# Kernel optimization log

Measured on AMD Instinct MI355X. Metric: run time of the kernel, lower is better.

Reference implementation:

```python
import jax, jax.numpy as jnp
import numpy as np

N_NODES = 100000
N_EDGES = 1600000
HID = 64
EDIM = 32


def _linear_params(key, fan_in, fan_out):
    # torch.nn.Linear default init: U(-1/sqrt(fan_in), 1/sqrt(fan_in))
    kw, kb = jax.random.split(key)
    bound = 1.0 / np.sqrt(fan_in)
    w = jax.random.uniform(kw, (fan_in, fan_out), jnp.float32, -bound, bound)
    b = jax.random.uniform(kb, (fan_out,), jnp.float32, -bound, bound)
    return w, b


def setup_inputs() -> dict:
    key = jax.random.key(0)
    ks = jax.random.split(key, 7)
    x = jax.random.normal(ks[0], (N_NODES, HID), jnp.float32)
    edge_index = jax.random.randint(ks[1], (2, N_EDGES), 0, N_NODES, jnp.int64)
    edge_attr = jax.random.normal(ks[2], (N_EDGES, EDIM), jnp.float32)
    ew1, eb1 = _linear_params(ks[3], 2 * HID + EDIM, HID)
    ew2, eb2 = _linear_params(ks[4], HID, HID)
    nw1, nb1 = _linear_params(ks[5], 2 * HID, HID)
    nw2, nb2 = _linear_params(ks[6], HID, HID)
    return {
        "x": x, "edge_index": edge_index, "edge_attr": edge_attr,
        "ew1": ew1, "eb1": eb1, "ew2": ew2, "eb2": eb2,
        "nw1": nw1, "nb1": nb1, "nw2": nw2, "nb2": nb2,
    }


def reference(x, edge_index, edge_attr, ew1, eb1, ew2, eb2, nw1, nb1, nw2, nb2):
    row, col = edge_index[0], edge_index[1]
    # gather endpoint features + edge attrs -> [E, 2*HID + EDIM]
    edge_features = jnp.concatenate([x[row], x[col], edge_attr], axis=-1)
    # edge MLP
    h = jax.nn.relu(edge_features @ ew1 + eb1)
    messages = h @ ew2 + eb2  # [E, HID]
    # scatter-add into source nodes (index_add_ on row)
    aggregated = jax.ops.segment_sum(messages, row, num_segments=x.shape[0])
    # node MLP
    out = jnp.concatenate([x, aggregated], axis=-1)
    out = jax.nn.relu(out @ nw1 + nb1)
    out = out @ nw2 + nb2
    return out
```

## Files before the change

kernel.cpp:

```cpp
#include <hip/hip_runtime.h>
#include <hip/hip_bf16.h>


#define TPB 256
#define MAXD 64
#define EDGE_BLOCKS 2048
#define SCAT_BLOCKS 2048
#define PREP_BLOCKS 1024
#define NODE_BLOCKS 1024

typedef float v2f __attribute__((ext_vector_type(2)));
typedef float v4f __attribute__((ext_vector_type(4)));
typedef __attribute__((ext_vector_type(8))) short s8v;
typedef __attribute__((ext_vector_type(4))) float f4v;
typedef __attribute__((ext_vector_type(4))) unsigned int u4v;
typedef unsigned int uint32;

#define SEG32(SRC, NCH, KB, W, COL, ACC)                                \
  for (int kc_ = 0; kc_ < (NCH); ++kc_) {                               \
    const float4 a_ = ((const float4*)(SRC))[kc_];                      \
    const float av_[4] = {a_.x, a_.y, a_.z, a_.w};                      \
    _Pragma("unroll")                                                   \
    for (int j_ = 0; j_ < 4; ++j_) {                                    \
      const float ak_ = av_[j_];                                        \
      const float* wr_ = (W) + ((KB) + kc_ * 4 + j_) * 64 + (COL);      \
      _Pragma("unroll")                                                 \
      for (int cc_ = 0; cc_ < 32; ++cc_)                                \
        ACC[cc_] = fmaf(ak_, wr_[cc_], ACC[cc_]);                       \
    }                                                                   \
  }

__device__ __forceinline__ uint32 pk_bf16(float a, float b) {
  uint32 ua = __float_as_uint(a);
  uint32 ub = __float_as_uint(b);
  ua = ua + 0x7FFFu + ((ua >> 16) & 1u);
  ub = ub + 0x7FFFu + ((ub >> 16) & 1u);
  return (ub & 0xFFFF0000u) | (ua >> 16);
}

__device__ __forceinline__ short f2bf(float f) {
  uint32 u = __float_as_uint(f);
  u = u + 0x7FFFu + ((u >> 16) & 1u);
  return (short)(u >> 16);
}


__global__ __launch_bounds__(TPB)
void k_scatter3(const int* __restrict__ ei, int* __restrict__ cnt,
                int2* __restrict__ ec, int E) {
  const int stride = gridDim.x * TPB;
  for (int e = blockIdx.x * TPB + threadIdx.x; e < E; e += stride) {
    const int r = ei[e];
    const int c = ei[E + e];
    int k = atomicAdd(&cnt[r], 1);
    if (k < MAXD) ec[(size_t)r * MAXD + k] = make_int2(e, c);
  }
}


__global__ __launch_bounds__(TPB)
void k_prep4(const float* __restrict__ x,
             const float* __restrict__ ew1, const float* __restrict__ eb1,
             float* __restrict__ U, float* __restrict__ V, int N)
{
  const int lane = threadIdx.x & 63;
  const int wid  = __builtin_amdgcn_readfirstlane(threadIdx.x >> 6);
  const int nunits = 4 * ((N + 63) / 64);
  const int wstride = gridDim.x * 4;

  for (int unit = blockIdx.x * 4 + wid; unit < nunits; unit += wstride) {
    const int q = unit & 3;
    const int n = (unit >> 2) * 64 + lane;
    if (n >= N) continue;

    const int uv = q >> 1;
    const int h = (q & 1) * 32;
    const float* W = ew1 + uv * 64 * 64;

    float acc[32];
    if (uv) {
      #pragma unroll
      for (int j = 0; j < 32; ++j) acc[j] = 0.f;
    } else {
      #pragma unroll
      for (int j = 0; j < 32; ++j) acc[j] = eb1[h + j];
    }
    SEG32(x + (size_t)n * 64, 16, 0, W, h, acc)

    float* dst = (uv ? V : U) + (size_t)n * 64 + h;
    float4* d4 = (float4*)dst;
    #pragma unroll
    for (int c4 = 0; c4 < 8; ++c4)
      d4[c4] = make_float4(acc[c4*4+0], acc[c4*4+1], acc[c4*4+2], acc[c4*4+3]);
  }
}


__global__ __launch_bounds__(TPB, 4)
void k_edge_mfma2(const float* __restrict__ U, const float* __restrict__ V,
                  const float* __restrict__ ea, const int2* __restrict__ ec,
                  const float* __restrict__ ew1,
                  const int* __restrict__ cnt,
                  float* __restrict__ H, int N)
{
  const int lane = threadIdx.x & 63;
  const int wid  = __builtin_amdgcn_readfirstlane(threadIdx.x >> 6);
  const int m16  = lane & 15;
  const int g4   = lane >> 4;

  s8v bfrag[4];
  #pragma unroll
  for (int t = 0; t < 4; ++t) {
    #pragma unroll
    for (int j = 0; j < 8; ++j)
      bfrag[t][j] = f2bf(ew1[(128 + g4 * 8 + j) * 64 + t * 16 + m16]);
  }
  asm volatile("" : "+v"(bfrag[0]), "+v"(bfrag[1]),
                    "+v"(bfrag[2]), "+v"(bfrag[3]));

  const int wstride = gridDim.x * 4;

  for (int n = blockIdx.x * 4 + wid; n < N; n += wstride) {
    int d = __builtin_amdgcn_readfirstlane(cnt[n]);
    d = (d < MAXD) ? d : MAXD;

    float uvv[4];
    #pragma unroll
    for (int t = 0; t < 4; ++t) uvv[t] = U[(size_t)n * 64 + t * 16 + m16];

    const int2* ecp = ec + (size_t)n * MAXD;
    float hs[4] = {0.f, 0.f, 0.f, 0.f};
    const int ntile = (d + 15) >> 4;

    for (int tile = 0; tile < ntile; ++tile) {
      const int sbase = tile * 16;

      const bool rowok = (sbase + m16) < d;
      const int eidr = rowok ? ecp[sbase + m16].x : 0;

      const float4* ear = (const float4*)(ea + (size_t)eidr * 32 + g4 * 8);
      const float4 fa = ear[0];
      const float4 fb = ear[1];
      u4v ua;
      ua.x = pk_bf16(fa.x, fa.y);
      ua.y = pk_bf16(fa.z, fa.w);
      ua.z = pk_bf16(fb.x, fb.y);
      ua.w = pk_bf16(fb.z, fb.w);
      const s8v afrag = __builtin_bit_cast(s8v, ua);

      const int4 c01 = *(const int4*)(ecp + sbase + g4 * 4);
      const int4 c23 = *(const int4*)(ecp + sbase + g4 * 4 + 2);
      const int ca[4] = {c01.y, c01.w, c23.y, c23.w};
      const int rg0 = sbase + g4 * 4;

      #pragma unroll
      for (int t = 0; t < 4; ++t) {
        f4v dd = __builtin_amdgcn_mfma_f32_16x16x32_bf16(
            afrag, bfrag[t], (f4v){0.f, 0.f, 0.f, 0.f}, 0, 0, 0);
        const int ch = t * 16 + m16;
        #pragma unroll
        for (int j = 0; j < 4; ++j) {
          const int rg = rg0 + j;
          const int cs = (rg < d) ? ca[j] : 0;
          const float vvv = V[(size_t)cs * 64 + ch];
          const float h = fmaxf(dd[j] + uvv[t] + vvv, 0.f);
          hs[t] += (rg < d) ? h : 0.f;
        }
      }
    }

    #pragma unroll
    for (int t = 0; t < 4; ++t) {
      hs[t] += __shfl_xor(hs[t], 16);
      hs[t] += __shfl_xor(hs[t], 32);
    }

    float hv = hs[0];
    hv = (g4 == 1) ? hs[1] : hv;
    hv = (g4 == 2) ? hs[2] : hv;
    hv = (g4 == 3) ? hs[3] : hv;
    H[(size_t)n * 64 + g4 * 16 + m16] = hv;
  }
}


__global__ __launch_bounds__(TPB)
void k_node4(const float* __restrict__ x, const float* __restrict__ Hin,
             const int* __restrict__ deg,
             const float* __restrict__ ew2, const float* __restrict__ eb2,
             const float* __restrict__ nw1, const float* __restrict__ nb1,
             const float* __restrict__ nw2, const float* __restrict__ nb2,
             float* __restrict__ out, int N)
{
  __shared__ float sb[2][64 * 65];

  const int tid  = threadIdx.x;
  const int wv   = __builtin_amdgcn_readfirstlane(tid >> 6);
  const int lane = tid & 63;
  const int grp  = wv >> 1;
  const int h    = (wv & 1) * 32;

  for (int base = blockIdx.x * 128; base < N; base += gridDim.x * 128) {
    const int n  = base + grp * 64 + lane;
    const bool valid = (n < N);
    const int nn = valid ? n : (N - 1);

    float* srow = &sb[grp][lane * 65];

    float acc[32];
    const float dg = (float)min(deg[nn], MAXD);
    #pragma unroll
    for (int j = 0; j < 32; ++j) acc[j] = dg * eb2[h + j];
    SEG32(Hin + (size_t)nn * 64, 16, 0, ew2, h, acc)

    #pragma unroll
    for (int j = 0; j < 32; ++j) srow[h + j] = acc[j];
    __syncthreads();

    float bcc[32];
    #pragma unroll
    for (int j = 0; j < 32; ++j) bcc[j] = nb1[h + j];
    SEG32(x + (size_t)nn * 64, 16, 0, nw1, h, bcc)
    for (int k = 0; k < 64; ++k) {
      const float ak = srow[k];
      const float* wr = nw1 + (64 + k) * 64 + h;
      #pragma unroll
      for (int cc = 0; cc < 32; ++cc) bcc[cc] = fmaf(ak, wr[cc], bcc[cc]);
    }
    __syncthreads();

    #pragma unroll
    for (int j = 0; j < 32; ++j) srow[h + j] = fmaxf(bcc[j], 0.f);
    __syncthreads();

    float occ[32];
    #pragma unroll
    for (int j = 0; j < 32; ++j) occ[j] = nb2[h + j];
    for (int k = 0; k < 64; ++k) {
      const float ak = srow[k];
      const float* wr = nw2 + k * 64 + h;
      #pragma unroll
      for (int cc = 0; cc < 32; ++cc) occ[cc] = fmaf(ak, wr[cc], occ[cc]);
    }

    if (valid) {
      float4* ov = (float4*)(out + (size_t)n * 64 + h);
      #pragma unroll
      for (int c4 = 0; c4 < 8; ++c4)
        ov[c4] = make_float4(occ[c4*4+0], occ[c4*4+1], occ[c4*4+2], occ[c4*4+3]);
    }
    __syncthreads();
  }
}


extern "C" void kernel_launch(void* const* d_in, const int* in_sizes, int n_in,
                              void* d_out, int out_size, void* d_ws, size_t ws_size,
                              hipStream_t stream) {
  const float* x   = (const float*)d_in[0];
  const int*   ei  = (const int*)d_in[1];
  const float* ea  = (const float*)d_in[2];
  const float* ew1 = (const float*)d_in[3];
  const float* eb1 = (const float*)d_in[4];
  const float* ew2 = (const float*)d_in[5];
  const float* eb2 = (const float*)d_in[6];
  const float* nw1 = (const float*)d_in[7];
  const float* nb1 = (const float*)d_in[8];
  const float* nw2 = (const float*)d_in[9];
  const float* nb2 = (const float*)d_in[10];
  float* out = (float*)d_out;

  const int N = in_sizes[0] / 64;
  const int E = in_sizes[1] / 2;

  float* U   = (float*)d_ws;
  float* V   = U + (size_t)N * 64;
  int* cnt   = (int*)(V + (size_t)N * 64);
  int2* ec   = (int2*)(cnt + N);
  float* H   = out;

  hipMemsetAsync(cnt, 0, (size_t)N * sizeof(int), stream);

  k_scatter3<<<SCAT_BLOCKS, TPB, 0, stream>>>(ei, cnt, ec, E);

  k_prep4<<<PREP_BLOCKS, TPB, 0, stream>>>(x, ew1, eb1, U, V, N);

  k_edge_mfma2<<<EDGE_BLOCKS, TPB, 0, stream>>>(
      U, V, ea, ec, ew1, cnt, H, N);

  k_node4<<<NODE_BLOCKS, TPB, 0, stream>>>(
      x, H, cnt, ew2, eb2, nw1, nb1, nw2, nb2, out, N);
}
```

Before: 325.2 us.

## Fuse edge bucketing scatter and U/V node precompute into one launch

Merges the edge bucketing kernel and the per-node U/V projection kernel into a single launch. Block roles are interleaved: two of every three blocks do the atomic scatter of edges into per-row buckets, and the third computes the U/V projections. The scatter loop also processes four edges per thread with loads and atomics batched to expose more memory parallelism. The aim is to overlap the atomic-heavy scatter with the compute-bound projection and save one launch, at the cost of role divergence within the grid.

Measured after the change: 316.8 us. 2.6% less time.

```diff
diff --git a/kernel.cpp b/kernel.cpp
--- a/kernel.cpp
+++ b/kernel.cpp
@@ -46,52 +46,75 @@
 
 
 __global__ __launch_bounds__(TPB)
-void k_scatter3(const int* __restrict__ ei, int* __restrict__ cnt,
-                int2* __restrict__ ec, int E) {
-  const int stride = gridDim.x * TPB;
-  for (int e = blockIdx.x * TPB + threadIdx.x; e < E; e += stride) {
-    const int r = ei[e];
-    const int c = ei[E + e];
-    int k = atomicAdd(&cnt[r], 1);
-    if (k < MAXD) ec[(size_t)r * MAXD + k] = make_int2(e, c);
-  }
-}
-
-
-__global__ __launch_bounds__(TPB)
-void k_prep4(const float* __restrict__ x,
-             const float* __restrict__ ew1, const float* __restrict__ eb1,
-             float* __restrict__ U, float* __restrict__ V, int N)
+void k_sp(const int* __restrict__ ei, int* __restrict__ cnt,
+          int2* __restrict__ ec,
+          const float* __restrict__ x,
+          const float* __restrict__ ew1, const float* __restrict__ eb1,
+          float* __restrict__ U, float* __restrict__ V,
+          int E, int N)
 {
-  const int lane = threadIdx.x & 63;
-  const int wid  = __builtin_amdgcn_readfirstlane(threadIdx.x >> 6);
-  const int nunits = 4 * ((N + 63) / 64);
-  const int wstride = gridDim.x * 4;
-
-  for (int unit = blockIdx.x * 4 + wid; unit < nunits; unit += wstride) {
-    const int q = unit & 3;
-    const int n = (unit >> 2) * 64 + lane;
-    if (n >= N) continue;
-
-    const int uv = q >> 1;
-    const int h = (q & 1) * 32;
-    const float* W = ew1 + uv * 64 * 64;
-
-    float acc[32];
-    if (uv) {
-      #pragma unroll
-      for (int j = 0; j < 32; ++j) acc[j] = 0.f;
-    } else {
-      #pragma unroll
-      for (int j = 0; j < 32; ++j) acc[j] = eb1[h + j];
-    }
-    SEG32(x + (size_t)n * 64, 16, 0, W, h, acc)
-
-    float* dst = (uv ? V : U) + (size_t)n * 64 + h;
-    float4* d4 = (float4*)dst;
-    #pragma unroll
-    for (int c4 = 0; c4 < 8; ++c4)
-      d4[c4] = make_float4(acc[c4*4+0], acc[c4*4+1], acc[c4*4+2], acc[c4*4+3]);
+  const int bid = blockIdx.x;
+  const int role = bid % 3;
+  const int tid = threadIdx.x;
+
+  if (role < 2) {
+    const int vid = (bid / 3) * 2 + role;
+    const int stride = SCAT_BLOCKS * TPB;
+    const int base = vid * TPB + tid;
+
+    for (int e0 = base; e0 < E; e0 += 4 * stride) {
+      int ee[4], rr[4], cc2[4], kk[4];
+      bool ok[4];
+      #pragma unroll
+      for (int j = 0; j < 4; ++j) {
+        ee[j] = e0 + j * stride;
+        ok[j] = ee[j] < E;
+      }
+      #pragma unroll
+      for (int j = 0; j < 4; ++j) {
+        rr[j]  = ok[j] ? ei[ee[j]]     : 0;
+        cc2[j] = ok[j] ? ei[E + ee[j]] : 0;
+      }
+      #pragma unroll
+      for (int j = 0; j < 4; ++j)
+        if (ok[j]) kk[j] = atomicAdd(&cnt[rr[j]], 1);
+      #pragma unroll
+      for (int j = 0; j < 4; ++j)
+        if (ok[j] && kk[j] < MAXD)
+          ec[(size_t)rr[j] * MAXD + kk[j]] = make_int2(ee[j], cc2[j]);
+    }
+  } else {
+    const int vid = bid / 3;
+    const int lane = tid & 63;
+    const int wid  = __builtin_amdgcn_readfirstlane(tid >> 6);
+    const int nunits = 4 * ((N + 63) / 64);
+    const int wstride = PREP_BLOCKS * 4;
+
+    for (int unit = vid * 4 + wid; unit < nunits; unit += wstride) {
+      const int q = unit & 3;
+      const int n = (unit >> 2) * 64 + lane;
+      if (n >= N) continue;
+
+      const int uv = q >> 1;
+      const int h = (q & 1) * 32;
+      const float* W = ew1 + uv * 64 * 64;
+
+      float acc[32];
+      if (uv) {
+        #pragma unroll
+        for (int j = 0; j < 32; ++j) acc[j] = 0.f;
+      } else {
+        #pragma unroll
+        for (int j = 0; j < 32; ++j) acc[j] = eb1[h + j];
+      }
+      SEG32(x + (size_t)n * 64, 16, 0, W, h, acc)
+
+      float* dst = (uv ? V : U) + (size_t)n * 64 + h;
+      float4* d4 = (float4*)dst;
+      #pragma unroll
+      for (int c4 = 0; c4 < 8; ++c4)
+        d4[c4] = make_float4(acc[c4*4+0], acc[c4*4+1], acc[c4*4+2], acc[c4*4+3]);
+    }
   }
 }
 
@@ -281,9 +304,8 @@
 
   hipMemsetAsync(cnt, 0, (size_t)N * sizeof(int), stream);
 
-  k_scatter3<<<SCAT_BLOCKS, TPB, 0, stream>>>(ei, cnt, ec, E);
-
-  k_prep4<<<PREP_BLOCKS, TPB, 0, stream>>>(x, ew1, eb1, U, V, N);
+  k_sp<<<3 * PREP_BLOCKS, TPB, 0, stream>>>(
+      ei, cnt, ec, x, ew1, eb1, U, V, E, N);
 
   k_edge_mfma2<<<EDGE_BLOCKS, TPB, 0, stream>>>(
       U, V, ea, ec, ew1, cnt, H, N);
```
